# Kernel tuning notes

Measured on AMD Instinct MI355X. Metric: run time of the kernel, lower is better.

Reference implementation:

```python
import jax, jax.numpy as jnp
import numpy as np

N, E = 50000, 800000
IN, HID, OUT = 128, 256, 128
BN_EPS = 1e-5


def setup_inputs() -> dict:
    key = jax.random.key(0)
    ks = jax.random.split(key, 12)
    x = jax.random.normal(ks[0], (N, IN), dtype=jnp.float32)
    edge_index = jax.random.randint(ks[1], (2, E), 0, N, dtype=jnp.int64)
    edge_weight = jax.random.uniform(ks[2], (E,), dtype=jnp.float32)
    # GCNConv weights (glorot-ish scale) and biases
    W0 = jax.random.normal(ks[3], (IN, HID), dtype=jnp.float32) * (1.0 / np.sqrt(IN))
    b0 = jnp.zeros((HID,), jnp.float32)
    W1 = jax.random.normal(ks[4], (HID, HID), dtype=jnp.float32) * (1.0 / np.sqrt(HID))
    b1 = jnp.zeros((HID,), jnp.float32)
    Wl = jax.random.normal(ks[5], (HID, OUT), dtype=jnp.float32) * (1.0 / np.sqrt(HID))
    bl = jnp.zeros((OUT,), jnp.float32)
    # BatchNorm affine params (eval mode: running_mean=0, running_var=1)
    g0 = 1.0 + 0.1 * jax.random.normal(ks[6], (HID,), dtype=jnp.float32)
    be0 = 0.1 * jax.random.normal(ks[7], (HID,), dtype=jnp.float32)
    g1 = 1.0 + 0.1 * jax.random.normal(ks[8], (HID,), dtype=jnp.float32)
    be1 = 0.1 * jax.random.normal(ks[9], (HID,), dtype=jnp.float32)
    return {"x": x, "edge_index": edge_index, "edge_weight": edge_weight,
            "W0": W0, "b0": b0, "W1": W1, "b1": b1, "Wl": Wl, "bl": bl,
            "g0": g0, "be0": be0, "g1": g1, "be1": be1}


def reference(x, edge_index, edge_weight, W0, b0, W1, b1, Wl, bl, g0, be0, g1, be1):
    n = x.shape[0]
    row, col = edge_index[0], edge_index[1]
    # add self-loops with weight 1 (GCNConv default)
    ar = jnp.arange(n)
    rowf = jnp.concatenate([row, ar])
    colf = jnp.concatenate([col, ar])
    wf = jnp.concatenate([edge_weight, jnp.ones((n,), x.dtype)])
    # symmetric normalization: D^{-1/2} A D^{-1/2}
    deg = jax.ops.segment_sum(wf, colf, num_segments=n)
    dinv = jnp.where(deg > 0, jax.lax.rsqrt(deg), 0.0)
    norm = dinv[rowf] * wf * dinv[colf]  # [E+N]

    def conv(h, W, b):
        h = h @ W                       # [n, d_out]
        msg = h[rowf] * norm[:, None]   # gather + scale per edge
        return jax.ops.segment_sum(msg, colf, num_segments=n) + b

    def bn_eval(h, g, b):
        # eval-mode BN with running_mean=0, running_var=1
        return h * (g / jnp.sqrt(1.0 + BN_EPS)) + b

    h = jax.nn.relu(bn_eval(conv(x, W0, b0), g0, be0))
    h = jax.nn.relu(bn_eval(conv(h, W1, b1), g1, be1))
    h = conv(h, Wl, bl)
    return jax.nn.log_softmax(h, axis=1)
```

## Files before the change

kernel.cpp:

```cpp
#include <hip/hip_runtime.h>
#include <cstddef>
#include <cstdint>


#define GCN_BN_EPS 1e-5f
#define NB_CHUNK 256

typedef short v8bf __attribute__((ext_vector_type(8)));
typedef float v4f __attribute__((ext_vector_type(4)));


__device__ __forceinline__ float4 unpack_bf4(uint2 u) {
  float4 r;
  r.x = __uint_as_float(u.x << 16);
  r.y = __uint_as_float(u.x & 0xffff0000u);
  r.z = __uint_as_float(u.y << 16);
  r.w = __uint_as_float(u.y & 0xffff0000u);
  return r;
}
__device__ __forceinline__ uint16_t f2bf(float f) {
  uint32_t u = __float_as_uint(f);
  return (uint16_t)((u + 0x7fffu + ((u >> 16) & 1u)) >> 16);
}
__device__ __forceinline__ uint2 pack_bf4(float4 v) {
  uint2 r;
  r.x = (uint32_t)f2bf(v.x) | ((uint32_t)f2bf(v.y) << 16);
  r.y = (uint32_t)f2bf(v.z) | ((uint32_t)f2bf(v.w) << 16);
  return r;
}


__global__ __launch_bounds__(256) void build_hist_kernel(
    const int* __restrict__ ei, const float* __restrict__ ew,
    int* __restrict__ col_, uint2* __restrict__ pk,
    unsigned int* __restrict__ histw, int E, int n) {
  extern __shared__ unsigned int h8[];
  __shared__ int s_flag;
  const int b = blockIdx.x;
  const int nw = (n + 3) >> 2;
  if (threadIdx.x == 0) {
    int nz = 0;
    for (int k = 1; k < 64; k += 2) nz |= ei[k];
    s_flag = (nz == 0) ? 1 : 0;
  }
  for (int i = threadIdx.x; i < nw; i += 256) h8[i] = 0u;
  __syncthreads();
  const int flag = s_flag;
  const int per = (E + NB_CHUNK - 1) / NB_CHUNK;
  const int e0 = b * per, e1 = min(e0 + per, E);
  for (int e = e0 + threadIdx.x; e < e1; e += 256) {
    int r, c;
    if (flag) { r = ei[2 * e]; c = ei[2 * (E + e)]; }
    else      { r = ei[e];     c = ei[E + e]; }
    col_[e] = c;
    pk[e] = make_uint2((unsigned)r, __float_as_uint(ew[e]));
    atomicAdd(&h8[c >> 2], 1u << ((c & 3) * 8));
  }
  __syncthreads();
  for (int i = threadIdx.x; i < nw; i += 256)
    histw[(size_t)b * nw + i] = h8[i];
}

__global__ __launch_bounds__(256) void scan1_conv_kernel(
    const unsigned int* __restrict__ histw, unsigned int* __restrict__ cntw,
    int* __restrict__ bsum, int nw, int nB,
    const float* __restrict__ x, uint16_t* __restrict__ xb,
    const float* __restrict__ W0, uint16_t* __restrict__ W0t,
    const float* __restrict__ W1, uint16_t* __restrict__ W1t,
    const float* __restrict__ Wl, uint16_t* __restrict__ Wlt,
    int t0, int convTot) {
  if (blockIdx.x >= nB) {
    int i = (blockIdx.x - nB) * 256 + threadIdx.x;
    if (i >= convTot) return;
    if (i < t0) {
      float4 v = *(const float4*)&x[(size_t)i * 4];
      *(uint2*)&xb[(size_t)i * 4] = pack_bf4(v);
      return;
    }
    int j = i - t0;
    if (j < 128 * 256) { int nn = j >> 7, k = j & 127; W0t[j] = f2bf(W0[(size_t)k * 256 + nn]); return; }
    j -= 128 * 256;
    if (j < 256 * 256) { int nn = j >> 8, k = j & 255; W1t[j] = f2bf(W1[(size_t)k * 256 + nn]); return; }
    j -= 256 * 256;
    if (j < 256 * 128) { int nn = j >> 8, k = j & 255; Wlt[j] = f2bf(Wl[(size_t)k * 128 + nn]); }
    return;
  }
  __shared__ int ws[4];
  const int j = blockIdx.x * 256 + threadIdx.x;
  unsigned int acc = 0;
  if (j < nw)
    for (int b = 0; b < NB_CHUNK; ++b) acc += histw[(size_t)b * nw + j];
  if (j < nw) cntw[j] = acc;
  int s = (int)((acc & 0xffu) + ((acc >> 8) & 0xffu) + ((acc >> 16) & 0xffu) + (acc >> 24));
  int x_ = s;
#pragma unroll
  for (int st = 1; st < 64; st <<= 1) x_ += __shfl_xor(x_, st, 64);
  if ((threadIdx.x & 63) == 0) ws[threadIdx.x >> 6] = x_;
  __syncthreads();
  if (threadIdx.x == 0) bsum[blockIdx.x] = ws[0] + ws[1] + ws[2] + ws[3];
}

__global__ __launch_bounds__(256) void scan3_base_kernel(
    const unsigned int* __restrict__ cntw, const int* __restrict__ bsum,
    int* __restrict__ off, unsigned int* __restrict__ histw,
    int nw, int nB, int n, int E) {
  __shared__ int wsum[4], woff[4];
  __shared__ int s_gbase;
  const int tid = threadIdx.x, lane = tid & 63, wv = tid >> 6;
  const int j = blockIdx.x * 256 + tid;
  unsigned int cw = (j < nw) ? cntw[j] : 0u;
  const int c0 = (int)(cw & 0xffu), c1 = (int)((cw >> 8) & 0xffu);
  const int c2 = (int)((cw >> 16) & 0xffu), c3 = (int)(cw >> 24);
  int s = c0 + c1 + c2 + c3;
  int x = s;
#pragma unroll
  for (int st = 1; st < 64; st <<= 1) { int t = __shfl_up(x, st, 64); if (lane >= st) x += t; }
  if (lane == 63) wsum[wv] = x;
  __syncthreads();
  if (tid == 0) { int r = 0; for (int k = 0; k < 4; ++k) { woff[k] = r; r += wsum[k]; } }
  if (wv == 0) {
    int v2 = (lane < nB) ? bsum[lane] : 0;
    int y = v2;
#pragma unroll
    for (int st = 1; st < 64; st <<= 1) { int t = __shfl_up(y, st, 64); if (lane >= st) y += t; }
    if (lane == blockIdx.x) s_gbase = y - v2;
  }
  __syncthreads();
  if (j < nw) {
    int excl = x - s + woff[wv] + s_gbase;
    uint4 o4;
    o4.x = excl; o4.y = excl + c0; o4.z = excl + c0 + c1; o4.w = excl + c0 + c1 + c2;
    *(uint4*)&off[4 * j] = o4;
    unsigned int run = 0;
    for (int b = 0; b < NB_CHUNK; ++b) {
      size_t idx = (size_t)b * nw + j;
      unsigned int w = histw[idx];
      histw[idx] = run;
      run += w;
    }
  }
  if (blockIdx.x == 0 && tid == 0) off[n] = E;
}

__global__ __launch_bounds__(256) void fill_kernel(
    const int* __restrict__ col_, const uint2* __restrict__ pk,
    const int* __restrict__ off, const unsigned int* __restrict__ histw,
    uint2* __restrict__ csr, int E, int n) {
  extern __shared__ unsigned int c8[];
  const int b = blockIdx.x;
  const int nw = (n + 3) >> 2;
  for (int i = threadIdx.x; i < nw; i += 256) c8[i] = 0u;
  __syncthreads();
  const int per = (E + NB_CHUNK - 1) / NB_CHUNK;
  const int e0 = b * per, e1 = min(e0 + per, E);
  const unsigned int* brel = histw + (size_t)b * nw;
  for (int e = e0 + threadIdx.x; e < e1; e += 256) {
    int c = col_[e];
    const int sh = (c & 3) * 8;
    unsigned old = atomicAdd(&c8[c >> 2], 1u << sh);
    int rel = (int)((old >> sh) & 0xffu) + (int)((brel[c >> 2] >> sh) & 0xffu);
    csr[off[c] + rel] = pk[e];
  }
}

__global__ void degdinv_kernel(const int* __restrict__ off, const uint2* __restrict__ csr,
                               float* __restrict__ dinv, int n) {
  int i = blockIdx.x * blockDim.x + threadIdx.x;
  if (i >= n) return;
  float s = 1.0f;
  int p1 = off[i + 1];
  for (int p = off[i]; p < p1; ++p) s += __uint_as_float(csr[p].y);
  dinv[i] = rsqrtf(s);
}


template <int EPI>
__global__ __launch_bounds__(256) void agg256_kernel(
    const uint16_t* __restrict__ hin, uint16_t* __restrict__ hout,
    const int* __restrict__ off, const uint2* __restrict__ csr,
    const float* __restrict__ dinv,
    const float* __restrict__ bias, const float* __restrict__ g,
    const float* __restrict__ be, int n) {
  const int lane = threadIdx.x & 63;
  const int c = blockIdx.x * 4 + (threadIdx.x >> 6);
  if (c >= n) return;
  const int f = lane * 4;
  const int e0 = off[c], e1 = off[c + 1];
  const float di = dinv[c];
  float4 self = unpack_bf4(*(const uint2*)&hin[(size_t)c * 256 + f]);
  float4 acc = make_float4(self.x * di, self.y * di, self.z * di, self.w * di);

  for (int base = e0; base < e1; base += 64) {
    int idx = base + lane;
    int rs = 0; float rv = 0.0f;
    if (idx < e1) {
      uint2 ev = csr[idx];
      rs = (int)ev.x;
      rv = dinv[rs] * __uint_as_float(ev.y);
    }
    const int m = min(64, e1 - base);
    const int nG = (m + 3) >> 2;
    for (int gI = 0; gI < nG; ++gI) {
      int e_ = gI * 4;
      int s0 = __shfl(rs, e_);     float v0 = __shfl(rv, e_);
      int s1 = __shfl(rs, e_ + 1); float v1 = __shfl(rv, e_ + 1);
      int sB = __shfl(rs, e_ + 2); float v2 = __shfl(rv, e_ + 2);
      int s3 = __shfl(rs, e_ + 3); float v3 = __shfl(rv, e_ + 3);
      float4 h0 = unpack_bf4(*(const uint2*)&hin[(size_t)s0 * 256 + f]);
      float4 h1 = unpack_bf4(*(const uint2*)&hin[(size_t)s1 * 256 + f]);
      float4 h2 = unpack_bf4(*(const uint2*)&hin[(size_t)sB * 256 + f]);
      float4 h3 = unpack_bf4(*(const uint2*)&hin[(size_t)s3 * 256 + f]);
      acc.x += v0 * h0.x + v1 * h1.x + v2 * h2.x + v3 * h3.x;
      acc.y += v0 * h0.y + v1 * h1.y + v2 * h2.y + v3 * h3.y;
      acc.z += v0 * h0.z + v1 * h1.z + v2 * h2.z + v3 * h3.z;
      acc.w += v0 * h0.w + v1 * h1.w + v2 * h2.w + v3 * h3.w;
    }
  }

  acc.x *= di; acc.y *= di; acc.z *= di; acc.w *= di;
  if (EPI == 1) {
    const float bns = rsqrtf(1.0f + GCN_BN_EPS);
    float4 bi = *(const float4*)&bias[f];
    float4 gi = *(const float4*)&g[f];
    float4 bei = *(const float4*)&be[f];
    acc.x = fmaxf((acc.x + bi.x) * gi.x * bns + bei.x, 0.0f);
    acc.y = fmaxf((acc.y + bi.y) * gi.y * bns + bei.y, 0.0f);
    acc.z = fmaxf((acc.z + bi.z) * gi.z * bns + bei.z, 0.0f);
    acc.w = fmaxf((acc.w + bi.w) * gi.w * bns + bei.w, 0.0f);
  }
  *(uint2*)&hout[(size_t)c * 256 + f] = pack_bf4(acc);
}

template <int EPI>
__global__ __launch_bounds__(256) void agg128_kernel(
    const uint16_t* __restrict__ hin, void* __restrict__ hout_,
    const int* __restrict__ off, const uint2* __restrict__ csr,
    const float* __restrict__ dinv,
    const float* __restrict__ bias, int n) {
  const int lane = threadIdx.x & 63;
  const int sub = lane & 31;
  const int hbase = lane & 32;
  const int c = blockIdx.x * 8 + (threadIdx.x >> 6) * 2 + (lane >> 5);
  const bool active = (c < n);
  const int f = sub * 4;

  int e0 = 0, e1 = 0;
  float di = 0.0f;
  float4 acc = make_float4(0.f, 0.f, 0.f, 0.f);
  if (active) {
    e0 = off[c]; e1 = off[c + 1];
    di = dinv[c];
    float4 self = unpack_bf4(*(const uint2*)&hin[(size_t)c * 128 + f]);
    acc = make_float4(self.x * di, self.y * di, self.z * di, self.w * di);
  }
  int nch = (e1 - e0 + 31) >> 5;
  nch = max(nch, __shfl(nch, lane ^ 32));

  for (int ch = 0; ch < nch; ++ch) {
    int idx = e0 + ch * 32 + sub;
    int rs = 0; float rv = 0.0f;
    if (active && idx < e1) {
      uint2 ev = csr[idx];
      rs = (int)ev.x;
      rv = dinv[rs] * __uint_as_float(ev.y);
    }
    int m = e1 - (e0 + ch * 32);
    m = m < 0 ? 0 : (m > 32 ? 32 : m);
    int mMax = max(m, __shfl(m, lane ^ 32));
    const int nG = (mMax + 3) >> 2;
    for (int gI = 0; gI < nG; ++gI) {
      int e_ = hbase + gI * 4;
      int s0 = __shfl(rs, e_);     float v0 = __shfl(rv, e_);
      int s1 = __shfl(rs, e_ + 1); float v1 = __shfl(rv, e_ + 1);
      int sB = __shfl(rs, e_ + 2); float v2 = __shfl(rv, e_ + 2);
      int s3 = __shfl(rs, e_ + 3); float v3 = __shfl(rv, e_ + 3);
      float4 h0 = unpack_bf4(*(const uint2*)&hin[(size_t)s0 * 128 + f]);
      float4 h1 = unpack_bf4(*(const uint2*)&hin[(size_t)s1 * 128 + f]);
      float4 h2 = unpack_bf4(*(const uint2*)&hin[(size_t)sB * 128 + f]);
      float4 h3 = unpack_bf4(*(const uint2*)&hin[(size_t)s3 * 128 + f]);
      acc.x += v0 * h0.x + v1 * h1.x + v2 * h2.x + v3 * h3.x;
      acc.y += v0 * h0.y + v1 * h1.y + v2 * h2.y + v3 * h3.y;
      acc.z += v0 * h0.z + v1 * h1.z + v2 * h2.z + v3 * h3.z;
      acc.w += v0 * h0.w + v1 * h1.w + v2 * h2.w + v3 * h3.w;
    }
  }

  acc.x *= di; acc.y *= di; acc.z *= di; acc.w *= di;
  if (EPI == 0) {
    uint16_t* hout = (uint16_t*)hout_;
    if (active) *(uint2*)&hout[(size_t)c * 128 + f] = pack_bf4(acc);
  } else {
    float* hout = (float*)hout_;
    float4 bi = active ? *(const float4*)&bias[f] : make_float4(0.f, 0.f, 0.f, 0.f);
    float tx = acc.x + bi.x, ty = acc.y + bi.y, tz = acc.z + bi.z, tw = acc.w + bi.w;
    float mx = fmaxf(fmaxf(tx, ty), fmaxf(tz, tw));
#pragma unroll
    for (int s = 1; s < 32; s <<= 1) mx = fmaxf(mx, __shfl_xor(mx, s, 64));
    float ex = expf(tx - mx) + expf(ty - mx) + expf(tz - mx) + expf(tw - mx);
#pragma unroll
    for (int s = 1; s < 32; s <<= 1) ex += __shfl_xor(ex, s, 64);
    float lse = logf(ex) + mx;
    if (active) {
      float4 res = make_float4(tx - lse, ty - lse, tz - lse, tw - lse);
      *(float4*)&hout[(size_t)c * 128 + f] = res;
    }
  }
}

template <int K, int NC, int EPI>
__global__ __launch_bounds__(256) void mfma_gemm_kernel(
    const uint16_t* __restrict__ A, const uint16_t* __restrict__ WT,
    uint16_t* __restrict__ Cb, int M, int tpb,
    const float* __restrict__ bias, const float* __restrict__ g,
    const float* __restrict__ be) {
  constexpr int CW = NC / 4;
  constexpr int NT = CW / 16;
  constexpr int KS = K / 32;
  const int lane = threadIdx.x & 63;
  const int wave = threadIdx.x >> 6;
  const int quad = lane >> 4;
  const int l16 = lane & 15;
  const int col0 = wave * CW;

  const int tiles = (M + 15) >> 4;
  int t0 = blockIdx.x * tpb;
  if (t0 >= tiles) return;
  int t1 = min(t0 + tpb, tiles);

  v8bf b[KS][NT];
#pragma unroll
  for (int ks = 0; ks < KS; ++ks)
#pragma unroll
    for (int nt = 0; nt < NT; ++nt)
      b[ks][nt] = *(const v8bf*)(WT + (size_t)(col0 + nt * 16 + l16) * K +
                                 ks * 32 + quad * 8);

  float sc[NT], o1[NT], o2[NT];
  if (EPI == 1) {
    const float bns = rsqrtf(1.0f + GCN_BN_EPS);
#pragma unroll
    for (int nt = 0; nt < NT; ++nt) {
      int col = col0 + nt * 16 + l16;
      sc[nt] = g[col] * bns; o1[nt] = bias[col]; o2[nt] = be[col];
    }
  }

  v8bf a[KS], an[KS];
  {
    int arow = min(t0 * 16 + l16, M - 1);
    const uint16_t* Ap = A + (size_t)arow * K + quad * 8;
#pragma unroll
    for (int ks = 0; ks < KS; ++ks) a[ks] = *(const v8bf*)(Ap + ks * 32);
  }
  for (int t = t0; t < t1; ++t) {
    if (t + 1 < t1) {
      int arow = min((t + 1) * 16 + l16, M - 1);
      const uint16_t* Ap = A + (size_t)arow * K + quad * 8;
#pragma unroll
      for (int ks = 0; ks < KS; ++ks) an[ks] = *(const v8bf*)(Ap + ks * 32);
    }
    v4f acc[NT];
#pragma unroll
    for (int nt = 0; nt < NT; ++nt) acc[nt] = (v4f){0.f, 0.f, 0.f, 0.f};
#pragma unroll
    for (int ks = 0; ks < KS; ++ks)
#pragma unroll
      for (int nt = 0; nt < NT; ++nt)
        acc[nt] = __builtin_amdgcn_mfma_f32_16x16x32_bf16(a[ks], b[ks][nt],
                                                          acc[nt], 0, 0, 0);
    const int row0 = t * 16 + quad * 4;
#pragma unroll
    for (int nt = 0; nt < NT; ++nt) {
      const int col = col0 + nt * 16 + l16;
#pragma unroll
      for (int r = 0; r < 4; ++r) {
        int row = row0 + r;
        if (row < M) {
          float v = acc[nt][r];
          if (EPI == 1) v = fmaxf((v + o1[nt]) * sc[nt] + o2[nt], 0.0f);
          Cb[(size_t)row * NC + col] = f2bf(v);
        }
      }
    }
#pragma unroll
    for (int ks = 0; ks < KS; ++ks) a[ks] = an[ks];
  }
}


static inline char* carve(char*& p, size_t bytes) {
  char* r = p;
  p += (bytes + 255) & ~(size_t)255;
  return r;
}

extern "C" void kernel_launch(void* const* d_in, const int* in_sizes, int n_in,
                              void* d_out, int out_size, void* d_ws, size_t ws_size,
                              hipStream_t stream) {
  const int N = in_sizes[0] / 128;
  const int E = in_sizes[2];

  const float* x  = (const float*)d_in[0];
  const int*   ei = (const int*)d_in[1];
  const float* ew = (const float*)d_in[2];
  const float* W0 = (const float*)d_in[3];
  const float* b0 = (const float*)d_in[4];
  const float* W1 = (const float*)d_in[5];
  const float* b1 = (const float*)d_in[6];
  const float* Wl = (const float*)d_in[7];
  const float* bl = (const float*)d_in[8];
  const float* g0 = (const float*)d_in[9];
  const float* be0 = (const float*)d_in[10];
  const float* g1 = (const float*)d_in[11];
  const float* be1 = (const float*)d_in[12];
  float* out = (float*)d_out;

  const int nw = (N + 3) / 4;

  char* p = (char*)d_ws;
  float*        dinv  = (float*)carve(p, (size_t)N * 4);
  unsigned int* cntw  = (unsigned int*)carve(p, (size_t)nw * 4);
  int*          off   = (int*)carve(p, (size_t)(N + 1) * 4);
  int*          bsum  = (int*)carve(p, 1024 * 4);
  int*          col_  = (int*)carve(p, (size_t)E * 4);
  uint2*        pk    = (uint2*)carve(p, (size_t)E * 8);
  uint2*        csr   = (uint2*)carve(p, (size_t)E * 8);
  unsigned int* histw = (unsigned int*)carve(p, (size_t)NB_CHUNK * nw * 4);
  uint16_t*     xb16  = (uint16_t*)carve(p, (size_t)N * 128 * 2);
  uint16_t*     bufR  = (uint16_t*)carve(p, (size_t)N * 128 * 2);
  uint16_t*     bufP  = (uint16_t*)carve(p, (size_t)N * 256 * 2);
  uint16_t*     bufQ  = (uint16_t*)carve(p, (size_t)N * 256 * 2);
  uint16_t*     W0t   = (uint16_t*)carve(p, (size_t)128 * 256 * 2);
  uint16_t*     W1t   = (uint16_t*)carve(p, (size_t)256 * 256 * 2);
  uint16_t*     Wlt   = (uint16_t*)carve(p, (size_t)256 * 128 * 2);

  const int TB = 256;
  const int gN = (N + TB - 1) / TB;
  const int gW4 = (N + 3) / 4;
  const int gW8 = (N + 7) / 8;
  const int tiles = (N + 15) / 16;
  const int TPB = 8;
  const int gG = (tiles + TPB - 1) / TPB;
  const size_t ldsU8 = (size_t)nw * 4;
  const int nB = (nw + 255) / 256;
  const int convT0 = N * 32;
  const int convTot = convT0 + 128 * 256 + 256 * 256 + 256 * 128;
  const int convB = (convTot + TB - 1) / TB;

  build_hist_kernel<<<NB_CHUNK, TB, ldsU8, stream>>>(ei, ew, col_, pk, histw, E, N);
  scan1_conv_kernel<<<nB + convB, TB, 0, stream>>>(histw, cntw, bsum, nw, nB,
                                                   x, xb16, W0, W0t, W1, W1t,
                                                   Wl, Wlt, convT0, convTot);
  scan3_base_kernel<<<nB, TB, 0, stream>>>(cntw, bsum, off, histw, nw, nB, N, E);
  fill_kernel<<<NB_CHUNK, TB, ldsU8, stream>>>(col_, pk, off, histw, csr, E, N);
  degdinv_kernel<<<gN, TB, 0, stream>>>(off, csr, dinv, N);

  agg128_kernel<0><<<gW8, 256, 0, stream>>>(xb16, bufR, off, csr, dinv, nullptr, N);
  mfma_gemm_kernel<128, 256, 1><<<gG, 256, 0, stream>>>(bufR, W0t, bufP, N, TPB,
                                                        b0, g0, be0);
  mfma_gemm_kernel<256, 256, 0><<<gG, 256, 0, stream>>>(bufP, W1t, bufQ, N, TPB,
                                                        nullptr, nullptr, nullptr);
  agg256_kernel<1><<<gW4, 256, 0, stream>>>(bufQ, bufP, off, csr, dinv,
                                            b1, g1, be1, N);
  mfma_gemm_kernel<256, 128, 0><<<gG, 256, 0, stream>>>(bufP, Wlt, bufR, N, TPB,
                                                        nullptr, nullptr, nullptr);
  agg128_kernel<2><<<gW8, 256, 0, stream>>>(bufR, out, off, csr, dinv, bl, N);
}
```

Before: 353.9 us.

## Compress CSR to packed 32-bit entries and use feature-chunked aggregation kernels

Degree is now accumulated with float atomics while the histogram is built, and dinv is computed in the conversion kernel, which removes the separate degdinv pass. The fill kernel precomputes dinv[src]*w and packs it as fp16 together with a 16-bit source index into one 32-bit CSR word, halving CSR traffic and dropping the per-edge dinv gather inside aggregation. The first two aggregations use a new kernel that splits the features into 8 chunks across blocks, so several nodes share a wavefront and gathers stay cache-friendly, with nontemporal loads and stores. The cost is fp16 precision on the edge norm, nondeterministic atomic degree sums, and a 16-bit index that only holds because N is 50000, below 65536.

```diff
diff --git a/kernel.cpp b/kernel.cpp
--- a/kernel.cpp
+++ b/kernel.cpp
@@ -28,12 +28,15 @@
   r.y = (uint32_t)f2bf(v.z) | ((uint32_t)f2bf(v.w) << 16);
   return r;
 }
+__device__ __forceinline__ float f16tof(unsigned int hi16) {
+  return (float)__builtin_bit_cast(_Float16, (unsigned short)hi16);
+}
 
 
 __global__ __launch_bounds__(256) void build_hist_kernel(
     const int* __restrict__ ei, const float* __restrict__ ew,
     int* __restrict__ col_, uint2* __restrict__ pk,
-    unsigned int* __restrict__ histw, int E, int n) {
+    unsigned int* __restrict__ histw, float* __restrict__ degw, int E, int n) {
   extern __shared__ unsigned int h8[];
   __shared__ int s_flag;
   const int b = blockIdx.x;
@@ -52,9 +55,11 @@
     int r, c;
     if (flag) { r = ei[2 * e]; c = ei[2 * (E + e)]; }
     else      { r = ei[e];     c = ei[E + e]; }
+    float w = ew[e];
     col_[e] = c;
-    pk[e] = make_uint2((unsigned)r, __float_as_uint(ew[e]));
+    pk[e] = make_uint2((unsigned)r, __float_as_uint(w));
     atomicAdd(&h8[c >> 2], 1u << ((c & 3) * 8));
+    atomicAdd(&degw[c], w);
   }
   __syncthreads();
   for (int i = threadIdx.x; i < nw; i += 256)
@@ -68,6 +73,7 @@
     const float* __restrict__ W0, uint16_t* __restrict__ W0t,
     const float* __restrict__ W1, uint16_t* __restrict__ W1t,
     const float* __restrict__ Wl, uint16_t* __restrict__ Wlt,
+    const float* __restrict__ degw, float* __restrict__ dinv,
     int t0, int convTot) {
   if (blockIdx.x >= nB) {
     int i = (blockIdx.x - nB) * 256 + threadIdx.x;
@@ -82,7 +88,9 @@
     j -= 128 * 256;
     if (j < 256 * 256) { int nn = j >> 8, k = j & 255; W1t[j] = f2bf(W1[(size_t)k * 256 + nn]); return; }
     j -= 256 * 256;
-    if (j < 256 * 128) { int nn = j >> 8, k = j & 255; Wlt[j] = f2bf(Wl[(size_t)k * 128 + nn]); }
+    if (j < 256 * 128) { int nn = j >> 8, k = j & 255; Wlt[j] = f2bf(Wl[(size_t)k * 128 + nn]); return; }
+    j -= 256 * 128;
+    dinv[j] = rsqrtf(1.0f + degw[j]);
     return;
   }
   __shared__ int ws[4];
@@ -145,7 +153,8 @@
 __global__ __launch_bounds__(256) void fill_kernel(
     const int* __restrict__ col_, const uint2* __restrict__ pk,
     const int* __restrict__ off, const unsigned int* __restrict__ histw,
-    uint2* __restrict__ csr, int E, int n) {
+    const float* __restrict__ dinv, unsigned int* __restrict__ csr4,
+    int E, int n) {
   extern __shared__ unsigned int c8[];
   const int b = blockIdx.x;
   const int nw = (n + 3) >> 2;
@@ -159,84 +168,78 @@
     const int sh = (c & 3) * 8;
     unsigned old = atomicAdd(&c8[c >> 2], 1u << sh);
     int rel = (int)((old >> sh) & 0xffu) + (int)((brel[c >> 2] >> sh) & 0xffu);
-    csr[off[c] + rel] = pk[e];
-  }
-}
-
-__global__ void degdinv_kernel(const int* __restrict__ off, const uint2* __restrict__ csr,
-                               float* __restrict__ dinv, int n) {
-  int i = blockIdx.x * blockDim.x + threadIdx.x;
-  if (i >= n) return;
-  float s = 1.0f;
-  int p1 = off[i + 1];
-  for (int p = off[i]; p < p1; ++p) s += __uint_as_float(csr[p].y);
-  dinv[i] = rsqrtf(s);
-}
-
-
-template <int EPI>
-__global__ __launch_bounds__(256) void agg256_kernel(
+    uint2 v = pk[e];
+    float nv = dinv[(int)v.x] * __uint_as_float(v.y);
+    unsigned short hb = __builtin_bit_cast(unsigned short, (_Float16)nv);
+    csr4[off[c] + rel] = (v.x & 0xffffu) | ((unsigned int)hb << 16);
+  }
+}
+
+
+template <int D, int CH, int SUB, int EPI>
+__global__ __launch_bounds__(256) void aggc_kernel(
     const uint16_t* __restrict__ hin, uint16_t* __restrict__ hout,
-    const int* __restrict__ off, const uint2* __restrict__ csr,
-    const float* __restrict__ dinv,
-    const float* __restrict__ bias, const float* __restrict__ g,
-    const float* __restrict__ be, int n) {
+    const int* __restrict__ off, const unsigned int* __restrict__ csr4,
+    const float* __restrict__ dinv, const float* __restrict__ bias,
+    const float* __restrict__ g, const float* __restrict__ be, int n) {
+  static_assert(D == CH * 8 && SUB * 4 == CH, "8 chunks, 4 feats/lane");
+  const int chunk = blockIdx.x & 7;
+  const int nblk = blockIdx.x >> 3;
+  constexpr int NPW = 64 / SUB;
   const int lane = threadIdx.x & 63;
-  const int c = blockIdx.x * 4 + (threadIdx.x >> 6);
+  const int ls = lane & (SUB - 1);
+  const int sb = lane & ~(SUB - 1);
+  const int c = (nblk * 4 + (threadIdx.x >> 6)) * NPW + (lane / SUB);
   if (c >= n) return;
-  const int f = lane * 4;
+  const int fo = chunk * CH + ls * 4;
+  const float di = dinv[c];
+  float4 acc = unpack_bf4(*(const uint2*)&hin[(size_t)c * D + fo]);
+  acc.x *= di; acc.y *= di; acc.z *= di; acc.w *= di;
   const int e0 = off[c], e1 = off[c + 1];
-  const float di = dinv[c];
-  float4 self = unpack_bf4(*(const uint2*)&hin[(size_t)c * 256 + f]);
-  float4 acc = make_float4(self.x * di, self.y * di, self.z * di, self.w * di);
-
-  for (int base = e0; base < e1; base += 64) {
-    int idx = base + lane;
-    int rs = 0; float rv = 0.0f;
-    if (idx < e1) {
-      uint2 ev = csr[idx];
-      rs = (int)ev.x;
-      rv = dinv[rs] * __uint_as_float(ev.y);
-    }
-    const int m = min(64, e1 - base);
-    const int nG = (m + 3) >> 2;
-    for (int gI = 0; gI < nG; ++gI) {
-      int e_ = gI * 4;
-      int s0 = __shfl(rs, e_);     float v0 = __shfl(rv, e_);
-      int s1 = __shfl(rs, e_ + 1); float v1 = __shfl(rv, e_ + 1);
-      int sB = __shfl(rs, e_ + 2); float v2 = __shfl(rv, e_ + 2);
-      int s3 = __shfl(rs, e_ + 3); float v3 = __shfl(rv, e_ + 3);
-      float4 h0 = unpack_bf4(*(const uint2*)&hin[(size_t)s0 * 256 + f]);
-      float4 h1 = unpack_bf4(*(const uint2*)&hin[(size_t)s1 * 256 + f]);
-      float4 h2 = unpack_bf4(*(const uint2*)&hin[(size_t)sB * 256 + f]);
-      float4 h3 = unpack_bf4(*(const uint2*)&hin[(size_t)s3 * 256 + f]);
-      acc.x += v0 * h0.x + v1 * h1.x + v2 * h2.x + v3 * h3.x;
-      acc.y += v0 * h0.y + v1 * h1.y + v2 * h2.y + v3 * h3.y;
-      acc.z += v0 * h0.z + v1 * h1.z + v2 * h2.z + v3 * h3.z;
-      acc.w += v0 * h0.w + v1 * h1.w + v2 * h2.w + v3 * h3.w;
-    }
-  }
-
+  for (int base = e0; base < e1; base += SUB) {
+    int idx = base + ls;
+    unsigned int ev = (idx < e1) ? __builtin_nontemporal_load(&csr4[idx]) : 0u;
+    const int m = min(SUB, e1 - base);
+    if (m == SUB) {
+#pragma unroll
+      for (int j = 0; j < SUB; ++j) {
+        unsigned int e = __shfl(ev, sb + j, 64);
+        float nv = f16tof(e >> 16);
+        float4 h = unpack_bf4(*(const uint2*)&hin[(size_t)(e & 0xffffu) * D + fo]);
+        acc.x += nv * h.x; acc.y += nv * h.y;
+        acc.z += nv * h.z; acc.w += nv * h.w;
+      }
+    } else {
+      for (int j = 0; j < m; ++j) {
+        unsigned int e = __shfl(ev, sb + j, 64);
+        float nv = f16tof(e >> 16);
+        float4 h = unpack_bf4(*(const uint2*)&hin[(size_t)(e & 0xffffu) * D + fo]);
+        acc.x += nv * h.x; acc.y += nv * h.y;
+        acc.z += nv * h.z; acc.w += nv * h.w;
+      }
+    }
+  }
   acc.x *= di; acc.y *= di; acc.z *= di; acc.w *= di;
   if (EPI == 1) {
     const float bns = rsqrtf(1.0f + GCN_BN_EPS);
-    float4 bi = *(const float4*)&bias[f];
-    float4 gi = *(const float4*)&g[f];
-    float4 bei = *(const float4*)&be[f];
+    float4 bi = *(const float4*)&bias[fo];
+    float4 gi = *(const float4*)&g[fo];
+    float4 bei = *(const float4*)&be[fo];
     acc.x = fmaxf((acc.x + bi.x) * gi.x * bns + bei.x, 0.0f);
     acc.y = fmaxf((acc.y + bi.y) * gi.y * bns + bei.y, 0.0f);
     acc.z = fmaxf((acc.z + bi.z) * gi.z * bns + bei.z, 0.0f);
     acc.w = fmaxf((acc.w + bi.w) * gi.w * bns + bei.w, 0.0f);
   }
-  *(uint2*)&hout[(size_t)c * 256 + f] = pack_bf4(acc);
+  uint2 pv = pack_bf4(acc);
+  unsigned long long v64 = (unsigned long long)pv.x | ((unsigned long long)pv.y << 32);
+  __builtin_nontemporal_store(v64, (unsigned long long*)&hout[(size_t)c * D + fo]);
 }
 
 template <int EPI>
 __global__ __launch_bounds__(256) void agg128_kernel(
     const uint16_t* __restrict__ hin, void* __restrict__ hout_,
-    const int* __restrict__ off, const uint2* __restrict__ csr,
-    const float* __restrict__ dinv,
-    const float* __restrict__ bias, int n) {
+    const int* __restrict__ off, const unsigned int* __restrict__ csr4,
+    const float* __restrict__ dinv, const float* __restrict__ bias, int n) {
   const int lane = threadIdx.x & 63;
   const int sub = lane & 31;
   const int hbase = lane & 32;
@@ -258,22 +261,22 @@
 
   for (int ch = 0; ch < nch; ++ch) {
     int idx = e0 + ch * 32 + sub;
-    int rs = 0; float rv = 0.0f;
-    if (active && idx < e1) {
-      uint2 ev = csr[idx];
-      rs = (int)ev.x;
-      rv = dinv[rs] * __uint_as_float(ev.y);
-    }
+    unsigned int ev = 0u;
+    if (active && idx < e1) ev = __builtin_nontemporal_load(&csr4[idx]);
     int m = e1 - (e0 + ch * 32);
     m = m < 0 ? 0 : (m > 32 ? 32 : m);
     int mMax = max(m, __shfl(m, lane ^ 32));
     const int nG = (mMax + 3) >> 2;
     for (int gI = 0; gI < nG; ++gI) {
       int e_ = hbase + gI * 4;
-      int s0 = __shfl(rs, e_);     float v0 = __shfl(rv, e_);
-      int s1 = __shfl(rs, e_ + 1); float v1 = __shfl(rv, e_ + 1);
-      int sB = __shfl(rs, e_ + 2); float v2 = __shfl(rv, e_ + 2);
-      int s3 = __shfl(rs, e_ + 3); float v3 = __shfl(rv, e_ + 3);
+      unsigned int ea = __shfl(ev, e_, 64);
+      unsigned int eb = __shfl(ev, e_ + 1, 64);
+      unsigned int ec = __shfl(ev, e_ + 2, 64);
+      unsigned int ed = __shfl(ev, e_ + 3, 64);
+      int s0 = (int)(ea & 0xffffu); float v0 = f16tof(ea >> 16);
+      int s1 = (int)(eb & 0xffffu); float v1 = f16tof(eb >> 16);
+      int sB = (int)(ec & 0xffffu); float v2 = f16tof(ec >> 16);
+      int s3 = (int)(ed & 0xffffu); float v3 = f16tof(ed >> 16);
       float4 h0 = unpack_bf4(*(const uint2*)&hin[(size_t)s0 * 128 + f]);
       float4 h1 = unpack_bf4(*(const uint2*)&hin[(size_t)s1 * 128 + f]);
       float4 h2 = unpack_bf4(*(const uint2*)&hin[(size_t)sB * 128 + f]);
@@ -419,12 +422,13 @@
 
   char* p = (char*)d_ws;
   float*        dinv  = (float*)carve(p, (size_t)N * 4);
+  float*        degw  = (float*)carve(p, (size_t)N * 4);
   unsigned int* cntw  = (unsigned int*)carve(p, (size_t)nw * 4);
   int*          off   = (int*)carve(p, (size_t)(N + 1) * 4);
   int*          bsum  = (int*)carve(p, 1024 * 4);
   int*          col_  = (int*)carve(p, (size_t)E * 4);
   uint2*        pk    = (uint2*)carve(p, (size_t)E * 8);
-  uint2*        csr   = (uint2*)carve(p, (size_t)E * 8);
+  unsigned int* csr4  = (unsigned int*)carve(p, (size_t)E * 4);
   unsigned int* histw = (unsigned int*)carve(p, (size_t)NB_CHUNK * nw * 4);
   uint16_t*     xb16  = (uint16_t*)carve(p, (size_t)N * 128 * 2);
   uint16_t*     bufR  = (uint16_t*)carve(p, (size_t)N * 128 * 2);
@@ -435,34 +439,38 @@
   uint16_t*     Wlt   = (uint16_t*)carve(p, (size_t)256 * 128 * 2);
 
   const int TB = 256;
-  const int gN = (N + TB - 1) / TB;
-  const int gW4 = (N + 3) / 4;
   const int gW8 = (N + 7) / 8;
+  const int nbA = (N + 63) / 64;
+  const int nbB = (N + 31) / 32;
   const int tiles = (N + 15) / 16;
   const int TPB = 8;
   const int gG = (tiles + TPB - 1) / TPB;
   const size_t ldsU8 = (size_t)nw * 4;
   const int nB = (nw + 255) / 256;
   const int convT0 = N * 32;
-  const int convTot = convT0 + 128 * 256 + 256 * 256 + 256 * 128;
+  const int convTot = convT0 + 128 * 256 + 256 * 256 + 256 * 128 + N;
   const int convB = (convTot + TB - 1) / TB;
 
-  build_hist_kernel<<<NB_CHUNK, TB, ldsU8, stream>>>(ei, ew, col_, pk, histw, E, N);
+  hipMemsetAsync(degw, 0, (size_t)N * 4, stream);
+  build_hist_kernel<<<NB_CHUNK, TB, ldsU8, stream>>>(ei, ew, col_, pk, histw,
+                                                     degw, E, N);
   scan1_conv_kernel<<<nB + convB, TB, 0, stream>>>(histw, cntw, bsum, nw, nB,
                                                    x, xb16, W0, W0t, W1, W1t,
-                                                   Wl, Wlt, convT0, convTot);
+                                                   Wl, Wlt, degw, dinv,
+                                                   convT0, convTot);
   scan3_base_kernel<<<nB, TB, 0, stream>>>(cntw, bsum, off, histw, nw, nB, N, E);
-  fill_kernel<<<NB_CHUNK, TB, ldsU8, stream>>>(col_, pk, off, histw, csr, E, N);
-  degdinv_kernel<<<gN, TB, 0, stream>>>(off, csr, dinv, N);
-
-  agg128_kernel<0><<<gW8, 256, 0, stream>>>(xb16, bufR, off, csr, dinv, nullptr, N);
+  fill_kernel<<<NB_CHUNK, TB, ldsU8, stream>>>(col_, pk, off, histw, dinv,
+                                               csr4, E, N);
+
+  aggc_kernel<128, 16, 4, 0><<<nbA * 8, 256, 0, stream>>>(
+      xb16, bufR, off, csr4, dinv, nullptr, nullptr, nullptr, N);
   mfma_gemm_kernel<128, 256, 1><<<gG, 256, 0, stream>>>(bufR, W0t, bufP, N, TPB,
                                                         b0, g0, be0);
   mfma_gemm_kernel<256, 256, 0><<<gG, 256, 0, stream>>>(bufP, W1t, bufQ, N, TPB,
                                                         nullptr, nullptr, nullptr);
-  agg256_kernel<1><<<gW4, 256, 0, stream>>>(bufQ, bufP, off, csr, dinv,
-                                            b1, g1, be1, N);
+  aggc_kernel<256, 32, 8, 1><<<nbB * 8, 256, 0, stream>>>(
+      bufQ, bufP, off, csr4, dinv, b1, g1, be1, N);
   mfma_gemm_kernel<256, 128, 0><<<gG, 256, 0, stream>>>(bufP, Wlt, bufR, N, TPB,
                                                         nullptr, nullptr, nullptr);
-  agg128_kernel<2><<<gW8, 256, 0, stream>>>(bufR, out, off, csr, dinv, bl, N);
-}
+  agg128_kernel<2><<<gW8, 256, 0, stream>>>(bufR, out, off, csr4, dinv, bl, N);
+}
```

Result: slower. 503.8 us (+42.4%).

## Pack CSR edges into 32-bit index+fp16 norm and simplify aggregation loops

Applied to the files above, without the earlier changes.

Adds a pass that precomputes per-edge dinv[src]*w, stores it as fp16 next to a 16-bit source index in one 32-bit word, and rewrites the aggregation kernels to read these packed entries directly. The old shuffle-based edge broadcast is replaced by scalar-uniform loads unrolled by 8. The 128-wide aggregation now uses one full wave per node with 2 features per lane. This halves CSR traffic and removes the per-edge dinv gather, at the cost of an extra kernel, fp16 precision for the edge weights, and a 16-bit index that only holds while N fits in 65536.

```diff
diff --git a/kernel.cpp b/kernel.cpp
--- a/kernel.cpp
+++ b/kernel.cpp
@@ -18,6 +18,8 @@
   r.w = __uint_as_float(u.y & 0xffff0000u);
   return r;
 }
+__device__ __forceinline__ float bflo(unsigned u) { return __uint_as_float(u << 16); }
+__device__ __forceinline__ float bfhi(unsigned u) { return __uint_as_float(u & 0xffff0000u); }
 __device__ __forceinline__ uint16_t f2bf(float f) {
   uint32_t u = __float_as_uint(f);
   return (uint16_t)((u + 0x7fffu + ((u >> 16) & 1u)) >> 16);
@@ -27,6 +29,13 @@
   r.x = (uint32_t)f2bf(v.x) | ((uint32_t)f2bf(v.y) << 16);
   r.y = (uint32_t)f2bf(v.z) | ((uint32_t)f2bf(v.w) << 16);
   return r;
+}
+__device__ __forceinline__ float f16tof(unsigned int hi16) {
+  return (float)__builtin_bit_cast(_Float16, (unsigned short)hi16);
+}
+__device__ __forceinline__ void fma_row4(float4& acc, float nv, uint2 u) {
+  acc.x += nv * bflo(u.x); acc.y += nv * bfhi(u.x);
+  acc.z += nv * bflo(u.y); acc.w += nv * bfhi(u.y);
 }
 
 
@@ -173,48 +182,60 @@
   dinv[i] = rsqrtf(s);
 }
 
+__global__ __launch_bounds__(256) void csr4conv_kernel(
+    const uint2* __restrict__ csr, const float* __restrict__ dinv,
+    unsigned int* __restrict__ csr4, int E) {
+  int e = blockIdx.x * 256 + threadIdx.x;
+  if (e >= E) return;
+  uint2 v = csr[e];
+  float nv = dinv[(int)v.x] * __uint_as_float(v.y);
+  unsigned short hb = __builtin_bit_cast(unsigned short, (_Float16)nv);
+  csr4[e] = (v.x & 0xffffu) | ((unsigned int)hb << 16);
+}
+
 
 template <int EPI>
-__global__ __launch_bounds__(256) void agg256_kernel(
+__global__ __launch_bounds__(256) void agg256s_kernel(
     const uint16_t* __restrict__ hin, uint16_t* __restrict__ hout,
-    const int* __restrict__ off, const uint2* __restrict__ csr,
+    const int* __restrict__ off, const unsigned int* __restrict__ csr4,
     const float* __restrict__ dinv,
     const float* __restrict__ bias, const float* __restrict__ g,
     const float* __restrict__ be, int n) {
   const int lane = threadIdx.x & 63;
-  const int c = blockIdx.x * 4 + (threadIdx.x >> 6);
+  const int c = __builtin_amdgcn_readfirstlane(blockIdx.x * 4 + (threadIdx.x >> 6));
   if (c >= n) return;
   const int f = lane * 4;
   const int e0 = off[c], e1 = off[c + 1];
   const float di = dinv[c];
-  float4 self = unpack_bf4(*(const uint2*)&hin[(size_t)c * 256 + f]);
-  float4 acc = make_float4(self.x * di, self.y * di, self.z * di, self.w * di);
-
-  for (int base = e0; base < e1; base += 64) {
-    int idx = base + lane;
-    int rs = 0; float rv = 0.0f;
-    if (idx < e1) {
-      uint2 ev = csr[idx];
-      rs = (int)ev.x;
-      rv = dinv[rs] * __uint_as_float(ev.y);
-    }
-    const int m = min(64, e1 - base);
-    const int nG = (m + 3) >> 2;
-    for (int gI = 0; gI < nG; ++gI) {
-      int e_ = gI * 4;
-      int s0 = __shfl(rs, e_);     float v0 = __shfl(rv, e_);
-      int s1 = __shfl(rs, e_ + 1); float v1 = __shfl(rv, e_ + 1);
-      int sB = __shfl(rs, e_ + 2); float v2 = __shfl(rv, e_ + 2);
-      int s3 = __shfl(rs, e_ + 3); float v3 = __shfl(rv, e_ + 3);
-      float4 h0 = unpack_bf4(*(const uint2*)&hin[(size_t)s0 * 256 + f]);
-      float4 h1 = unpack_bf4(*(const uint2*)&hin[(size_t)s1 * 256 + f]);
-      float4 h2 = unpack_bf4(*(const uint2*)&hin[(size_t)sB * 256 + f]);
-      float4 h3 = unpack_bf4(*(const uint2*)&hin[(size_t)s3 * 256 + f]);
-      acc.x += v0 * h0.x + v1 * h1.x + v2 * h2.x + v3 * h3.x;
-      acc.y += v0 * h0.y + v1 * h1.y + v2 * h2.y + v3 * h3.y;
-      acc.z += v0 * h0.z + v1 * h1.z + v2 * h2.z + v3 * h3.z;
-      acc.w += v0 * h0.w + v1 * h1.w + v2 * h2.w + v3 * h3.w;
-    }
+  const uint16_t* __restrict__ hrow = hin + (size_t)c * 256;
+  float4 acc = unpack_bf4(*(const uint2*)&hrow[f]);
+  acc.x *= di; acc.y *= di; acc.z *= di; acc.w *= di;
+
+  int e = e0;
+  for (; e + 8 <= e1; e += 8) {
+    unsigned v0 = csr4[e + 0], v1 = csr4[e + 1], v2 = csr4[e + 2], v3 = csr4[e + 3];
+    unsigned v4 = csr4[e + 4], v5 = csr4[e + 5], v6 = csr4[e + 6], v7 = csr4[e + 7];
+    uint2 h0 = *(const uint2*)&hin[(size_t)(v0 & 0xffffu) * 256 + f];
+    uint2 h1 = *(const uint2*)&hin[(size_t)(v1 & 0xffffu) * 256 + f];
+    uint2 h2 = *(const uint2*)&hin[(size_t)(v2 & 0xffffu) * 256 + f];
+    uint2 h3 = *(const uint2*)&hin[(size_t)(v3 & 0xffffu) * 256 + f];
+    uint2 h4 = *(const uint2*)&hin[(size_t)(v4 & 0xffffu) * 256 + f];
+    uint2 h5 = *(const uint2*)&hin[(size_t)(v5 & 0xffffu) * 256 + f];
+    uint2 h6 = *(const uint2*)&hin[(size_t)(v6 & 0xffffu) * 256 + f];
+    uint2 h7 = *(const uint2*)&hin[(size_t)(v7 & 0xffffu) * 256 + f];
+    fma_row4(acc, f16tof(v0 >> 16), h0);
+    fma_row4(acc, f16tof(v1 >> 16), h1);
+    fma_row4(acc, f16tof(v2 >> 16), h2);
+    fma_row4(acc, f16tof(v3 >> 16), h3);
+    fma_row4(acc, f16tof(v4 >> 16), h4);
+    fma_row4(acc, f16tof(v5 >> 16), h5);
+    fma_row4(acc, f16tof(v6 >> 16), h6);
+    fma_row4(acc, f16tof(v7 >> 16), h7);
+  }
+  for (; e < e1; ++e) {
+    unsigned v = csr4[e];
+    uint2 h = *(const uint2*)&hin[(size_t)(v & 0xffffu) * 256 + f];
+    fma_row4(acc, f16tof(v >> 16), h);
   }
 
   acc.x *= di; acc.y *= di; acc.z *= di; acc.w *= di;
@@ -232,78 +253,65 @@
 }
 
 template <int EPI>
-__global__ __launch_bounds__(256) void agg128_kernel(
+__global__ __launch_bounds__(256) void agg128s_kernel(
     const uint16_t* __restrict__ hin, void* __restrict__ hout_,
-    const int* __restrict__ off, const uint2* __restrict__ csr,
-    const float* __restrict__ dinv,
-    const float* __restrict__ bias, int n) {
+    const int* __restrict__ off, const unsigned int* __restrict__ csr4,
+    const float* __restrict__ dinv, const float* __restrict__ bias, int n) {
   const int lane = threadIdx.x & 63;
-  const int sub = lane & 31;
-  const int hbase = lane & 32;
-  const int c = blockIdx.x * 8 + (threadIdx.x >> 6) * 2 + (lane >> 5);
-  const bool active = (c < n);
-  const int f = sub * 4;
-
-  int e0 = 0, e1 = 0;
-  float di = 0.0f;
-  float4 acc = make_float4(0.f, 0.f, 0.f, 0.f);
-  if (active) {
-    e0 = off[c]; e1 = off[c + 1];
-    di = dinv[c];
-    float4 self = unpack_bf4(*(const uint2*)&hin[(size_t)c * 128 + f]);
-    acc = make_float4(self.x * di, self.y * di, self.z * di, self.w * di);
-  }
-  int nch = (e1 - e0 + 31) >> 5;
-  nch = max(nch, __shfl(nch, lane ^ 32));
-
-  for (int ch = 0; ch < nch; ++ch) {
-    int idx = e0 + ch * 32 + sub;
-    int rs = 0; float rv = 0.0f;
-    if (active && idx < e1) {
-      uint2 ev = csr[idx];
-      rs = (int)ev.x;
-      rv = dinv[rs] * __uint_as_float(ev.y);
-    }
-    int m = e1 - (e0 + ch * 32);
-    m = m < 0 ? 0 : (m > 32 ? 32 : m);
-    int mMax = max(m, __shfl(m, lane ^ 32));
-    const int nG = (mMax + 3) >> 2;
-    for (int gI = 0; gI < nG; ++gI) {
-      int e_ = hbase + gI * 4;
-      int s0 = __shfl(rs, e_);     float v0 = __shfl(rv, e_);
-      int s1 = __shfl(rs, e_ + 1); float v1 = __shfl(rv, e_ + 1);
-      int sB = __shfl(rs, e_ + 2); float v2 = __shfl(rv, e_ + 2);
-      int s3 = __shfl(rs, e_ + 3); float v3 = __shfl(rv, e_ + 3);
-      float4 h0 = unpack_bf4(*(const uint2*)&hin[(size_t)s0 * 128 + f]);
-      float4 h1 = unpack_bf4(*(const uint2*)&hin[(size_t)s1 * 128 + f]);
-      float4 h2 = unpack_bf4(*(const uint2*)&hin[(size_t)sB * 128 + f]);
-      float4 h3 = unpack_bf4(*(const uint2*)&hin[(size_t)s3 * 128 + f]);
-      acc.x += v0 * h0.x + v1 * h1.x + v2 * h2.x + v3 * h3.x;
-      acc.y += v0 * h0.y + v1 * h1.y + v2 * h2.y + v3 * h3.y;
-      acc.z += v0 * h0.z + v1 * h1.z + v2 * h2.z + v3 * h3.z;
-      acc.w += v0 * h0.w + v1 * h1.w + v2 * h2.w + v3 * h3.w;
-    }
-  }
-
-  acc.x *= di; acc.y *= di; acc.z *= di; acc.w *= di;
+  const int c = __builtin_amdgcn_readfirstlane(blockIdx.x * 4 + (threadIdx.x >> 6));
+  if (c >= n) return;
+  const int f = lane * 2;
+  const int e0 = off[c], e1 = off[c + 1];
+  const float di = dinv[c];
+  unsigned su = *(const unsigned*)&hin[(size_t)c * 128 + f];
+  float a0 = bflo(su) * di, a1 = bfhi(su) * di;
+
+  int e = e0;
+  for (; e + 8 <= e1; e += 8) {
+    unsigned v0 = csr4[e + 0], v1 = csr4[e + 1], v2 = csr4[e + 2], v3 = csr4[e + 3];
+    unsigned v4 = csr4[e + 4], v5 = csr4[e + 5], v6 = csr4[e + 6], v7 = csr4[e + 7];
+    unsigned h0 = *(const unsigned*)&hin[(size_t)(v0 & 0xffffu) * 128 + f];
+    unsigned h1 = *(const unsigned*)&hin[(size_t)(v1 & 0xffffu) * 128 + f];
+    unsigned h2 = *(const unsigned*)&hin[(size_t)(v2 & 0xffffu) * 128 + f];
+    unsigned h3 = *(const unsigned*)&hin[(size_t)(v3 & 0xffffu) * 128 + f];
+    unsigned h4 = *(const unsigned*)&hin[(size_t)(v4 & 0xffffu) * 128 + f];
+    unsigned h5 = *(const unsigned*)&hin[(size_t)(v5 & 0xffffu) * 128 + f];
+    unsigned h6 = *(const unsigned*)&hin[(size_t)(v6 & 0xffffu) * 128 + f];
+    unsigned h7 = *(const unsigned*)&hin[(size_t)(v7 & 0xffffu) * 128 + f];
+    float n0 = f16tof(v0 >> 16), n1 = f16tof(v1 >> 16);
+    float n2 = f16tof(v2 >> 16), n3 = f16tof(v3 >> 16);
+    float n4 = f16tof(v4 >> 16), n5 = f16tof(v5 >> 16);
+    float n6 = f16tof(v6 >> 16), n7 = f16tof(v7 >> 16);
+    a0 += n0 * bflo(h0) + n1 * bflo(h1) + n2 * bflo(h2) + n3 * bflo(h3);
+    a1 += n0 * bfhi(h0) + n1 * bfhi(h1) + n2 * bfhi(h2) + n3 * bfhi(h3);
+    a0 += n4 * bflo(h4) + n5 * bflo(h5) + n6 * bflo(h6) + n7 * bflo(h7);
+    a1 += n4 * bfhi(h4) + n5 * bfhi(h5) + n6 * bfhi(h6) + n7 * bfhi(h7);
+  }
+  for (; e < e1; ++e) {
+    unsigned v = csr4[e];
+    unsigned h = *(const unsigned*)&hin[(size_t)(v & 0xffffu) * 128 + f];
+    float nv = f16tof(v >> 16);
+    a0 += nv * bflo(h); a1 += nv * bfhi(h);
+  }
+
+  a0 *= di; a1 *= di;
   if (EPI == 0) {
     uint16_t* hout = (uint16_t*)hout_;
-    if (active) *(uint2*)&hout[(size_t)c * 128 + f] = pack_bf4(acc);
+    unsigned pv = (unsigned)f2bf(a0) | ((unsigned)f2bf(a1) << 16);
+    *(unsigned*)&hout[(size_t)c * 128 + f] = pv;
   } else {
     float* hout = (float*)hout_;
-    float4 bi = active ? *(const float4*)&bias[f] : make_float4(0.f, 0.f, 0.f, 0.f);
-    float tx = acc.x + bi.x, ty = acc.y + bi.y, tz = acc.z + bi.z, tw = acc.w + bi.w;
-    float mx = fmaxf(fmaxf(tx, ty), fmaxf(tz, tw));
-#pragma unroll
-    for (int s = 1; s < 32; s <<= 1) mx = fmaxf(mx, __shfl_xor(mx, s, 64));
-    float ex = expf(tx - mx) + expf(ty - mx) + expf(tz - mx) + expf(tw - mx);
-#pragma unroll
-    for (int s = 1; s < 32; s <<= 1) ex += __shfl_xor(ex, s, 64);
+    float2 bi = *(const float2*)&bias[f];
+    float t0 = a0 + bi.x, t1 = a1 + bi.y;
+    float mx = fmaxf(t0, t1);
+#pragma unroll
+    for (int s = 1; s < 64; s <<= 1) mx = fmaxf(mx, __shfl_xor(mx, s, 64));
+    float ex = expf(t0 - mx) + expf(t1 - mx);
+#pragma unroll
+    for (int s = 1; s < 64; s <<= 1) ex += __shfl_xor(ex, s, 64);
     float lse = logf(ex) + mx;
-    if (active) {
-      float4 res = make_float4(tx - lse, ty - lse, tz - lse, tw - lse);
-      *(float4*)&hout[(size_t)c * 128 + f] = res;
-    }
+    float2 res = make_float2(t0 - lse, t1 - lse);
+    *(float2*)&hout[(size_t)c * 128 + f] = res;
   }
 }
 
@@ -433,11 +441,12 @@
   uint16_t*     W0t   = (uint16_t*)carve(p, (size_t)128 * 256 * 2);
   uint16_t*     W1t   = (uint16_t*)carve(p, (size_t)256 * 256 * 2);
   uint16_t*     Wlt   = (uint16_t*)carve(p, (size_t)256 * 128 * 2);
+  unsigned int* csr4  = (unsigned int*)col_;
 
   const int TB = 256;
   const int gN = (N + TB - 1) / TB;
   const int gW4 = (N + 3) / 4;
-  const int gW8 = (N + 7) / 8;
+  const int gE = (E + TB - 1) / TB;
   const int tiles = (N + 15) / 16;
   const int TPB = 8;
   const int gG = (tiles + TPB - 1) / TPB;
@@ -454,15 +463,17 @@
   scan3_base_kernel<<<nB, TB, 0, stream>>>(cntw, bsum, off, histw, nw, nB, N, E);
   fill_kernel<<<NB_CHUNK, TB, ldsU8, stream>>>(col_, pk, off, histw, csr, E, N);
   degdinv_kernel<<<gN, TB, 0, stream>>>(off, csr, dinv, N);
-
-  agg128_kernel<0><<<gW8, 256, 0, stream>>>(xb16, bufR, off, csr, dinv, nullptr, N);
+  csr4conv_kernel<<<gE, TB, 0, stream>>>(csr, dinv, csr4, E);
+
+  agg128s_kernel<0><<<gW4, 256, 0, stream>>>(xb16, bufR, off, csr4, dinv,
+                                             nullptr, N);
   mfma_gemm_kernel<128, 256, 1><<<gG, 256, 0, stream>>>(bufR, W0t, bufP, N, TPB,
                                                         b0, g0, be0);
   mfma_gemm_kernel<256, 256, 0><<<gG, 256, 0, stream>>>(bufP, W1t, bufQ, N, TPB,
                                                         nullptr, nullptr, nullptr);
-  agg256_kernel<1><<<gW4, 256, 0, stream>>>(bufQ, bufP, off, csr, dinv,
-                                            b1, g1, be1, N);
+  agg256s_kernel<1><<<gW4, 256, 0, stream>>>(bufQ, bufP, off, csr4, dinv,
+                                             b1, g1, be1, N);
   mfma_gemm_kernel<256, 128, 0><<<gG, 256, 0, stream>>>(bufP, Wlt, bufR, N, TPB,
                                                         nullptr, nullptr, nullptr);
-  agg128_kernel<2><<<gW8, 256, 0, stream>>>(bufR, out, off, csr, dinv, bl, N);
-}
+  agg128s_kernel<2><<<gW4, 256, 0, stream>>>(bufR, out, off, csr4, dinv, bl, N);
+}
```

Result: slower. 362.0 us (+2.3%).
